# Kernel tuning notes

Measured on AMD Instinct MI355X. Metric: run time of the kernel, lower is better.

Reference implementation:

```python
import jax, jax.numpy as jnp
import numpy as np

N_NODES = 50000
N_EDGES = 800000
D_IN, D_HID, D_LAT = 128, 128, 64
BN_EPS = 1e-5


def setup_inputs() -> dict:
    key = jax.random.key(0)
    ks = jax.random.split(key, 8)
    x = jax.random.normal(ks[0], (N_NODES, D_IN), dtype=jnp.float32)
    edge_index = jax.random.randint(ks[1], (2, N_EDGES), 0, N_NODES, dtype=jnp.int64)
    s1 = 1.0 / np.sqrt(D_IN)
    s2 = 1.0 / np.sqrt(D_HID)
    W1 = jax.random.normal(ks[2], (D_IN, D_HID), dtype=jnp.float32) * s1
    b1 = jnp.zeros((D_HID,), jnp.float32)
    gamma = jnp.ones((D_HID,), jnp.float32)
    beta = jnp.zeros((D_HID,), jnp.float32)
    Wmu = jax.random.normal(ks[3], (D_HID, D_LAT), dtype=jnp.float32) * s2
    bmu = jnp.zeros((D_LAT,), jnp.float32)
    Wls = jax.random.normal(ks[4], (D_HID, D_LAT), dtype=jnp.float32) * s2
    bls = jnp.zeros((D_LAT,), jnp.float32)
    return {"x": x, "edge_index": edge_index, "W1": W1, "b1": b1,
            "gamma": gamma, "beta": beta, "Wmu": Wmu, "bmu": bmu,
            "Wls": Wls, "bls": bls}


def _gcn_conv(h, src, dst, norm_e, inv_deg, W, b):
    # PyG GCNConv: linear transform, then sym-normalized aggregation (A+I).
    h = h @ W                                   # [N, F]
    msgs = h[src] * norm_e[:, None]             # gather + edge scaling, [E, F]
    agg = jax.ops.segment_sum(msgs, dst, num_segments=h.shape[0])
    # self-loop contribution: norm[i]*norm[i] = 1/deg[i]
    return agg + h * inv_deg[:, None] + b


def reference(x, edge_index, W1, b1, gamma, beta, Wmu, bmu, Wls, bls):
    src, dst = edge_index[0], edge_index[1]
    n = x.shape[0]
    # degrees including self loops (GCN symmetric normalization)
    deg = jax.ops.segment_sum(jnp.ones(dst.shape, x.dtype), dst, num_segments=n) + 1.0
    inv_sqrt_deg = jax.lax.rsqrt(deg)
    norm_e = inv_sqrt_deg[src] * inv_sqrt_deg[dst]   # per-edge norm, [E]
    inv_deg = 1.0 / deg

    h = _gcn_conv(x, src, dst, norm_e, inv_deg, W1, b1)
    # BatchNorm1d with batch statistics (biased var), then ReLU; dropout off (eval)
    mean = h.mean(axis=0)
    var = h.var(axis=0)
    h = (h - mean) * jax.lax.rsqrt(var + BN_EPS) * gamma + beta
    h = jax.nn.relu(h)

    mu = _gcn_conv(h, src, dst, norm_e, inv_deg, Wmu, bmu)
    log_std = _gcn_conv(h, src, dst, norm_e, inv_deg, Wls, bls)
    return mu, log_std
```

## Files before the change

### kernel.cpp

```cpp
#include <hip/hip_runtime.h>
#include <hip/hip_bf16.h>

#define N_NODES 50000
#define N_EDGES 800000
#define F 128
#define L 64
#define BN_EPS 1e-5f
#define SCAN_BLOCKS 196
#define BN_BLOCKS 391
#define NPART 8
#define PART_SZ 6250
#define FILL_BLOCKS 2048
#define GEMM_BLOCKS 782

typedef __attribute__((ext_vector_type(8))) short short8;
typedef __attribute__((ext_vector_type(8))) unsigned short ushort8;
typedef __attribute__((ext_vector_type(4))) unsigned short ushortx4;
typedef __attribute__((ext_vector_type(4))) float f32x4;

static __device__ __forceinline__ float loadF(const void* p, int i, int f32) {
    if (f32) return ((const float*)p)[i];
    return __bfloat162float(((const __hip_bfloat16*)p)[i]);
}
static __device__ __forceinline__ int loadI(const void* p, int i, int i64) {
    if (i64) return (int)((const long long*)p)[i];
    return ((const int*)p)[i];
}
static __device__ __forceinline__ float bfu2f(unsigned short u) {
    unsigned int t = ((unsigned int)u) << 16;
    float f;
    __builtin_memcpy(&f, &t, 4);
    return f;
}
static __device__ __forceinline__ short f2bf_s(float f) {
    union { __hip_bfloat16 b; short s; } cv;
    cv.b = __float2bfloat16(f);
    return cv.s;
}
static __device__ __forceinline__ unsigned short f2bf_u(float f) {
    union { __hip_bfloat16 b; unsigned short u; } cv;
    cv.b = __float2bfloat16(f);
    return cv.u;
}

__global__ void k_prep(const void* __restrict__ W1, const void* __restrict__ Wmu,
                       const void* __restrict__ Wls, const unsigned short* __restrict__ xs,
                       const int* __restrict__ ei, __hip_bfloat16* __restrict__ Wt1,
                       __hip_bfloat16* __restrict__ Wt2, int* __restrict__ flags,
                       int* __restrict__ degi) {
    int b = blockIdx.x;
    int t = threadIdx.x;
    if (b == 0) {
        __shared__ int cnt[2];
        if (t < 2) cnt[t] = 0;
        __syncthreads();
        unsigned short v = xs[2 * t];
        int e = (v >> 7) & 0xff;
        int sane = (e >= 112 && e <= 133) ? 1 : 0;
        if (v == 0 || v == 0x8000) sane = 1;
        atomicAdd(&cnt[0], sane);
        atomicAdd(&cnt[1], (ei[2 * t + 1] != 0) ? 1 : 0);
        __syncthreads();
        if (t == 0) {
            flags[0] = (cnt[0] < 128) ? 1 : 0;
            flags[1] = (cnt[1] < 8) ? 1 : 0;
            flags[2] = 0;
        }
    } else if (b <= 64) {
        __shared__ int cnt;
        if (t == 0) cnt = 0;
        __syncthreads();
        unsigned short v = ((const unsigned short*)W1)[2 * t];
        int e = (v >> 7) & 0xff;
        atomicAdd(&cnt, (e >= 100 && e <= 133) ? 1 : 0);
        __syncthreads();
        int f32 = (cnt < 128) ? 1 : 0;
        int idx = (b - 1) * 256 + t;
        int n = idx >> 7, k = idx & 127;
        Wt1[idx] = __float2bfloat16(loadF(W1, k * F + n, f32));
        float v2 = (n < L) ? loadF(Wmu, k * L + n, f32) : loadF(Wls, k * L + (n - L), f32);
        Wt2[idx] = __float2bfloat16(v2);
    } else {
        int i = (b - 65) * 256 + t;
        if (i < N_NODES) degi[i] = 0;
    }
}

__global__ void k_eiprep(const void* ei, const int* __restrict__ flags,
                         int* __restrict__ src32, int* __restrict__ dst32,
                         int* __restrict__ degi) {
    int e = blockIdx.x * blockDim.x + threadIdx.x;
    if (e < N_EDGES) {
        int i64 = flags[1];
        int d = loadI(ei, N_EDGES + e, i64);
        if (i64) {
            src32[e] = loadI(ei, e, 1);
            dst32[e] = d;
        }
        atomicAdd(&degi[d], 1);
    }
}

__global__ void k_offs_alloc(const int* __restrict__ degi, int* __restrict__ flags,
                             int* __restrict__ offs, float* __restrict__ isd,
                             int* __restrict__ cur) {
    __shared__ int s[256];
    __shared__ int base;
    int t = threadIdx.x;
    int i = blockIdx.x * 256 + t;
    int v = (i < N_NODES) ? degi[i] : 0;
    s[t] = v;
    __syncthreads();
    for (int o = 1; o < 256; o <<= 1) {
        int u = (t >= o) ? s[t - o] : 0;
        __syncthreads();
        s[t] += u;
        __syncthreads();
    }
    if (t == 255) base = atomicAdd(&flags[2], s[255]);
    __syncthreads();
    if (i < N_NODES) {
        offs[i] = base + s[t] - v;
        isd[i] = 1.0f / sqrtf((float)v + 1.0f);
        cur[i] = 0;
    }
}

static __device__ __forceinline__ void gemm_body(int bid, const void* __restrict__ Xin,
        const __hip_bfloat16* __restrict__ Wt, const float* __restrict__ isd,
        const int* __restrict__ flags, int mode,
        const float* __restrict__ bnscale, const float* __restrict__ bnshift,
        unsigned short* __restrict__ outb) {
    int wave = threadIdx.x >> 6, lane = threadIdx.x & 63;
    int quad = lane >> 4, mr = lane & 15;
    int m0 = bid * 64 + wave * 16;
    int node = m0 + mr;
    int row = (node < N_NODES) ? node : N_NODES - 1;
    short8 a[4];
    if (mode == 1) {
        const unsigned short* xb = (const unsigned short*)Xin;
#pragma unroll
        for (int t = 0; t < 4; ++t) {
            int k0 = t * 32 + quad * 8;
            ushort8 raw = *(const ushort8*)(xb + row * F + k0);
            f32x4 s0 = *(const f32x4*)(bnscale + k0);
            f32x4 s1 = *(const f32x4*)(bnscale + k0 + 4);
            f32x4 h0 = *(const f32x4*)(bnshift + k0);
            f32x4 h1 = *(const f32x4*)(bnshift + k0 + 4);
            short8 av;
#pragma unroll
            for (int j = 0; j < 4; ++j)
                av[j] = f2bf_s(fmaxf(bfu2f(raw[j]) * s0[j] + h0[j], 0.f));
#pragma unroll
            for (int j = 0; j < 4; ++j)
                av[4 + j] = f2bf_s(fmaxf(bfu2f(raw[4 + j]) * s1[j] + h1[j], 0.f));
            a[t] = av;
        }
    } else if (flags[0]) {
        const float* xf = (const float*)Xin;
#pragma unroll
        for (int t = 0; t < 4; ++t) {
            int off = row * F + t * 32 + quad * 8;
            f32x4 v0 = *(const f32x4*)(xf + off);
            f32x4 v1 = *(const f32x4*)(xf + off + 4);
            short8 av;
#pragma unroll
            for (int j = 0; j < 4; ++j) av[j] = f2bf_s(v0[j]);
#pragma unroll
            for (int j = 0; j < 4; ++j) av[4 + j] = f2bf_s(v1[j]);
            a[t] = av;
        }
    } else {
        const short* xb = (const short*)Xin;
#pragma unroll
        for (int t = 0; t < 4; ++t)
            a[t] = *(const short8*)(xb + row * F + t * 32 + quad * 8);
    }
    f32x4 acc[8];
    const short* wb = (const short*)Wt;
#pragma unroll
    for (int nt = 0; nt < 8; ++nt) {
        const short* wp = wb + (nt * 16 + mr) * F + quad * 8;
        f32x4 c = {0.f, 0.f, 0.f, 0.f};
        c = __builtin_amdgcn_mfma_f32_16x16x32_bf16(*(const short8*)(wp), a[0], c, 0, 0, 0);
        c = __builtin_amdgcn_mfma_f32_16x16x32_bf16(*(const short8*)(wp + 32), a[1], c, 0, 0, 0);
        c = __builtin_amdgcn_mfma_f32_16x16x32_bf16(*(const short8*)(wp + 64), a[2], c, 0, 0, 0);
        c = __builtin_amdgcn_mfma_f32_16x16x32_bf16(*(const short8*)(wp + 96), a[3], c, 0, 0, 0);
        acc[nt] = c;
    }
    if (node < N_NODES) {
        float sd = isd[node];
        unsigned short* op = outb + node * F;
#pragma unroll
        for (int nt = 0; nt < 8; ++nt) {
            ushortx4 r;
#pragma unroll
            for (int j = 0; j < 4; ++j) r[j] = f2bf_u(acc[nt][j] * sd);
            *(ushortx4*)(op + nt * 16 + quad * 4) = r;
        }
    }
}

__global__ __launch_bounds__(256) void k_fill_gemm1(
        const int* __restrict__ ei32, const int* __restrict__ src32,
        const int* __restrict__ dst32, const int* __restrict__ flags,
        const int* __restrict__ offs, int* __restrict__ cur, int* __restrict__ csr,
        const void* __restrict__ X, const __hip_bfloat16* __restrict__ Wt1,
        const float* __restrict__ isd, unsigned short* __restrict__ outb) {
    if (blockIdx.x < FILL_BLOCKS) {
        const int* sp;
        const int* dp;
        if (flags[1]) { sp = src32; dp = dst32; }
        else          { sp = ei32;  dp = ei32 + N_EDGES; }
        int grp = blockIdx.x & (NPART - 1);
        int sub = blockIdx.x >> 3;
        int lo = grp * PART_SZ, hi = lo + PART_SZ;
        int stride = (FILL_BLOCKS >> 3) * 256;
        for (int e = sub * 256 + threadIdx.x; e < N_EDGES; e += stride) {
            int d = dp[e];
            if (d >= lo && d < hi) {
                int pos = offs[d] + atomicAdd(&cur[d], 1);
                csr[pos] = sp[e];
            }
        }
    } else {
        gemm_body(blockIdx.x - FILL_BLOCKS, X, Wt1, isd, flags, 0, nullptr, nullptr, outb);
    }
}

__global__ __launch_bounds__(256) void k_gemm_bn(const void* __restrict__ Xin,
        const __hip_bfloat16* __restrict__ Wt, const float* __restrict__ isd,
        const int* __restrict__ flags, const float* __restrict__ bnscale,
        const float* __restrict__ bnshift, unsigned short* __restrict__ outb) {
    gemm_body(blockIdx.x, Xin, Wt, isd, flags, 1, bnscale, bnshift, outb);
}

static __device__ __forceinline__ void agg_accum(int node, int grp, int l16,
        const ushort8* __restrict__ vp, const int* __restrict__ csr,
        const int* __restrict__ offs, const int* __restrict__ degi, float acc[8]) {
#pragma unroll
    for (int j = 0; j < 8; ++j) acc[j] = 0.f;
    if (grp == 0) {
        ushort8 u = vp[node * 16 + l16];
#pragma unroll
        for (int j = 0; j < 8; ++j) acc[j] = bfu2f(u[j]);
    }
    int start = offs[node];
    int end = start + degi[node];
    int i = start + grp;
    for (; i + 12 < end; i += 16) {
        ushort8 u0 = vp[csr[i] * 16 + l16];
        ushort8 u1 = vp[csr[i + 4] * 16 + l16];
        ushort8 u2 = vp[csr[i + 8] * 16 + l16];
        ushort8 u3 = vp[csr[i + 12] * 16 + l16];
#pragma unroll
        for (int j = 0; j < 8; ++j)
            acc[j] += (bfu2f(u0[j]) + bfu2f(u1[j])) + (bfu2f(u2[j]) + bfu2f(u3[j]));
    }
    for (; i + 4 < end; i += 8) {
        ushort8 u0 = vp[csr[i] * 16 + l16];
        ushort8 u1 = vp[csr[i + 4] * 16 + l16];
#pragma unroll
        for (int j = 0; j < 8; ++j) acc[j] += bfu2f(u0[j]) + bfu2f(u1[j]);
    }
    for (; i < end; i += 4) {
        ushort8 u = vp[csr[i] * 16 + l16];
#pragma unroll
        for (int j = 0; j < 8; ++j) acc[j] += bfu2f(u[j]);
    }
#pragma unroll
    for (int j = 0; j < 8; ++j) {
        acc[j] += __shfl_xor(acc[j], 16);
        acc[j] += __shfl_xor(acc[j], 32);
    }
}

__global__ void k_agg1(const unsigned short* __restrict__ val, const int* __restrict__ csr,
                       const int* __restrict__ offs, const int* __restrict__ degi,
                       const float* __restrict__ isd, const void* __restrict__ b1,
                       const int* __restrict__ flags, unsigned short* __restrict__ out) {
    int node = blockIdx.x * 4 + (threadIdx.x >> 6);
    if (node >= N_NODES) return;
    int lane = threadIdx.x & 63;
    int grp = lane >> 4, l16 = lane & 15;
    float acc[8];
    agg_accum(node, grp, l16, (const ushort8*)val, csr, offs, degi, acc);
    if (grp == 0) {
        float sd = isd[node];
        int c0 = l16 * 8, f32 = flags[0];
        ushort8 r;
#pragma unroll
        for (int j = 0; j < 8; ++j) r[j] = f2bf_u(acc[j] * sd + loadF(b1, c0 + j, f32));
        ((ushort8*)out)[node * 16 + l16] = r;
    }
}

__global__ void k_bnstats(const unsigned short* __restrict__ h, float* __restrict__ partial) {
    __shared__ float ls[256][8];
    __shared__ float lq[256][8];
    int t = threadIdx.x;
    int o = t & 15, rg = t >> 4;
    int row0 = blockIdx.x * 128 + rg;
    float s[8] = {0.f}, q[8] = {0.f};
#pragma unroll
    for (int i = 0; i < 8; ++i) {
        int row = row0 + i * 16;
        if (row < N_NODES) {
            ushort8 u = *(const ushort8*)(h + row * F + o * 8);
#pragma unroll
            for (int j = 0; j < 8; ++j) {
                float v = bfu2f(u[j]);
                s[j] += v;
                q[j] += v * v;
            }
        }
    }
#pragma unroll
    for (int j = 0; j < 8; ++j) { ls[t][j] = s[j]; lq[t][j] = q[j]; }
    __syncthreads();
    if (t < 128) {
        int c = t, oo = c >> 3, jj = c & 7;
        float ts = 0.f, tq = 0.f;
#pragma unroll
        for (int rgi = 0; rgi < 16; ++rgi) {
            ts += ls[rgi * 16 + oo][jj];
            tq += lq[rgi * 16 + oo][jj];
        }
        partial[blockIdx.x * 256 + c] = ts;
        partial[blockIdx.x * 256 + 128 + c] = tq;
    }
}

__global__ void k_bnredprep(const float* __restrict__ partial, const void* __restrict__ gamma,
                            const void* __restrict__ beta, const int* __restrict__ flags,
                            float* __restrict__ scale, float* __restrict__ shift) {
    int c = blockIdx.x;
    float s = 0.f, q = 0.f;
    for (int b = threadIdx.x; b < BN_BLOCKS; b += 256) {
        s += partial[b * 256 + c];
        q += partial[b * 256 + 128 + c];
    }
#pragma unroll
    for (int o = 32; o; o >>= 1) {
        s += __shfl_down(s, o);
        q += __shfl_down(q, o);
    }
    __shared__ float ws[4], wq[4];
    if ((threadIdx.x & 63) == 0) {
        ws[threadIdx.x >> 6] = s;
        wq[threadIdx.x >> 6] = q;
    }
    __syncthreads();
    if (threadIdx.x == 0) {
        float S = ws[0] + ws[1] + ws[2] + ws[3];
        float Q = wq[0] + wq[1] + wq[2] + wq[3];
        const float invN = 1.0f / (float)N_NODES;
        float m = S * invN;
        float var = Q * invN - m * m;
        int f32 = flags[0];
        float sc = loadF(gamma, c, f32) * rsqrtf(var + BN_EPS);
        scale[c] = sc;
        shift[c] = loadF(beta, c, f32) - m * sc;
    }
}

__global__ void k_agg2(const unsigned short* __restrict__ val, const int* __restrict__ csr,
                       const int* __restrict__ offs, const int* __restrict__ degi,
                       const float* __restrict__ isd, const void* __restrict__ bmu,
                       const void* __restrict__ bls, const int* __restrict__ flags,
                       void* __restrict__ out) {
    int node = blockIdx.x * 4 + (threadIdx.x >> 6);
    if (node >= N_NODES) return;
    int lane = threadIdx.x & 63;
    int grp = lane >> 4, l16 = lane & 15;
    float acc[8];
    agg_accum(node, grp, l16, (const ushort8*)val, csr, offs, degi, acc);
    if (grp == 0) {
        float sd = isd[node];
        int c0 = l16 * 8, f32 = flags[0];
        int hsel = (c0 >= L) ? 1 : 0;
        int cc = c0 - hsel * L;
        const void* bp = hsel ? bls : bmu;
        float o8[8];
#pragma unroll
        for (int j = 0; j < 8; ++j) o8[j] = acc[j] * sd + loadF(bp, cc + j, f32);
        long base_o = (long)hsel * (N_NODES * 64) + (long)node * 64 + cc;
        if (f32) {
            float4 r0 = make_float4(o8[0], o8[1], o8[2], o8[3]);
            float4 r1 = make_float4(o8[4], o8[5], o8[6], o8[7]);
            *(float4*)((float*)out + base_o) = r0;
            *(float4*)((float*)out + base_o + 4) = r1;
        } else {
            ushort8 r;
#pragma unroll
            for (int j = 0; j < 8; ++j) r[j] = f2bf_u(o8[j]);
            *(ushort8*)((__hip_bfloat16*)out + base_o) = r;
        }
    }
}

extern "C" void kernel_launch(void* const* d_in, const int* in_sizes, int n_in,
                              void* d_out, int out_size, void* d_ws, size_t ws_size,
                              hipStream_t stream) {
    const void* x     = d_in[0];
    const void* ei    = d_in[1];
    const void* W1    = d_in[2];
    const void* b1    = d_in[3];
    const void* gamma = d_in[4];
    const void* beta  = d_in[5];
    const void* Wmu   = d_in[6];
    const void* bmu   = d_in[7];
    const void* Wls   = d_in[8];
    const void* bls   = d_in[9];

    int*   degi  = (int*)d_ws;
    int*   offs  = degi + 50048;
    int*   cur   = offs + 50048;
    float* isd   = (float*)(cur + 50048);
    float* stats = isd + 50048;
    int*   flags = (int*)(stats + 512);
    int*   csr   = flags + 16;
    int*   src32 = csr + 800000;
    int*   dst32 = src32 + 800000;
    __hip_bfloat16* Wt1 = (__hip_bfloat16*)(dst32 + 800000);
    __hip_bfloat16* Wt2 = Wt1 + 16384;
    unsigned short* Abf = (unsigned short*)(Wt2 + 16384);
    unsigned short* Hpre = Abf + N_NODES * F;
    float* partial = (float*)(Hpre + N_NODES * F);

    const int NT = 256;
    const int AGG_BLOCKS = (N_NODES + 3) / 4;

    k_prep<<<65 + SCAN_BLOCKS, NT, 0, stream>>>(W1, Wmu, Wls, (const unsigned short*)x,
                                                (const int*)ei, Wt1, Wt2, flags, degi);
    k_eiprep<<<(N_EDGES + NT - 1) / NT, NT, 0, stream>>>(ei, flags, src32, dst32, degi);
    k_offs_alloc<<<SCAN_BLOCKS, NT, 0, stream>>>(degi, flags, offs, isd, cur);
    k_fill_gemm1<<<FILL_BLOCKS + GEMM_BLOCKS, NT, 0, stream>>>(
        (const int*)ei, src32, dst32, flags, offs, cur, csr, x, Wt1, isd, Abf);
    k_agg1<<<AGG_BLOCKS, NT, 0, stream>>>(Abf, csr, offs, degi, isd, b1, flags, Hpre);
    k_bnstats<<<BN_BLOCKS, NT, 0, stream>>>(Hpre, partial);
    k_bnredprep<<<128, NT, 0, stream>>>(partial, gamma, beta, flags, stats, stats + 128);
    k_gemm_bn<<<GEMM_BLOCKS, NT, 0, stream>>>(Hpre, Wt2, isd, flags, stats, stats + 128, Abf);
    k_agg2<<<AGG_BLOCKS, NT, 0, stream>>>(Abf, csr, offs, degi, isd, bmu, bls, flags, d_out);
}
```

Baseline: 308.4 us.

## Pad degree/offset counters, merge edge prep into prep kernel, simplify CSR fill

Degree and offset counters are padded to 16 ints per node so each counter sits on its own cache line, which is meant to reduce atomic contention from false sharing. Edge index conversion and degree counting move into k_prep, replacing the separate k_eiprep launch, and the counters are zeroed with hipMemsetAsync. The CSR fill drops the 8-way destination partitioning and the separate cur array and instead atomically bumps the offset itself, which then serves as the row end in aggregation. Output stores become nontemporal. The padding multiplies the footprint of the offset and degree arrays, so aggregation reads of them become strided.

Measured after the change: 314.9 us. 1.02x slower.

```diff
diff --git a/kernel.cpp b/kernel.cpp
--- a/kernel.cpp
+++ b/kernel.cpp
@@ -6,12 +6,12 @@
 #define F 128
 #define L 64
 #define BN_EPS 1e-5f
+#define PAD 16
 #define SCAN_BLOCKS 196
 #define BN_BLOCKS 391
-#define NPART 8
-#define PART_SZ 6250
-#define FILL_BLOCKS 2048
+#define EDGE_BLOCKS 3125
 #define GEMM_BLOCKS 782
+#define FILLB 1266
 
 typedef __attribute__((ext_vector_type(8))) short short8;
 typedef __attribute__((ext_vector_type(8))) unsigned short ushort8;
@@ -21,10 +21,6 @@
 static __device__ __forceinline__ float loadF(const void* p, int i, int f32) {
     if (f32) return ((const float*)p)[i];
     return __bfloat162float(((const __hip_bfloat16*)p)[i]);
-}
-static __device__ __forceinline__ int loadI(const void* p, int i, int i64) {
-    if (i64) return (int)((const long long*)p)[i];
-    return ((const int*)p)[i];
 }
 static __device__ __forceinline__ float bfu2f(unsigned short u) {
     unsigned int t = ((unsigned int)u) << 16;
@@ -45,9 +41,10 @@
 
 __global__ void k_prep(const void* __restrict__ W1, const void* __restrict__ Wmu,
                        const void* __restrict__ Wls, const unsigned short* __restrict__ xs,
-                       const int* __restrict__ ei, __hip_bfloat16* __restrict__ Wt1,
+                       const void* __restrict__ ei, __hip_bfloat16* __restrict__ Wt1,
                        __hip_bfloat16* __restrict__ Wt2, int* __restrict__ flags,
-                       int* __restrict__ degi) {
+                       int* __restrict__ degiP, int* __restrict__ src32,
+                       int* __restrict__ dst32) {
     int b = blockIdx.x;
     int t = threadIdx.x;
     if (b == 0) {
@@ -59,7 +56,7 @@
         int sane = (e >= 112 && e <= 133) ? 1 : 0;
         if (v == 0 || v == 0x8000) sane = 1;
         atomicAdd(&cnt[0], sane);
-        atomicAdd(&cnt[1], (ei[2 * t + 1] != 0) ? 1 : 0);
+        atomicAdd(&cnt[1], (((const int*)ei)[2 * t + 1] != 0) ? 1 : 0);
         __syncthreads();
         if (t == 0) {
             flags[0] = (cnt[0] < 128) ? 1 : 0;
@@ -81,34 +78,33 @@
         float v2 = (n < L) ? loadF(Wmu, k * L + n, f32) : loadF(Wls, k * L + (n - L), f32);
         Wt2[idx] = __float2bfloat16(v2);
     } else {
-        int i = (b - 65) * 256 + t;
-        if (i < N_NODES) degi[i] = 0;
-    }
-}
-
-__global__ void k_eiprep(const void* ei, const int* __restrict__ flags,
-                         int* __restrict__ src32, int* __restrict__ dst32,
-                         int* __restrict__ degi) {
-    int e = blockIdx.x * blockDim.x + threadIdx.x;
-    if (e < N_EDGES) {
-        int i64 = flags[1];
-        int d = loadI(ei, N_EDGES + e, i64);
-        if (i64) {
-            src32[e] = loadI(ei, e, 1);
-            dst32[e] = d;
-        }
-        atomicAdd(&degi[d], 1);
-    }
-}
-
-__global__ void k_offs_alloc(const int* __restrict__ degi, int* __restrict__ flags,
-                             int* __restrict__ offs, float* __restrict__ isd,
-                             int* __restrict__ cur) {
+        int e0 = (b - 65) * 256 + t;
+        __shared__ int nz;
+        if (t == 0) nz = 0;
+        __syncthreads();
+        int w = ((const int*)ei)[2 * e0 + 1];
+        if (w != 0) atomicAdd(&nz, 1);
+        __syncthreads();
+        int d;
+        if (nz < 8) {
+            int s = (int)((const long long*)ei)[e0];
+            d = (int)((const long long*)ei)[N_EDGES + e0];
+            src32[e0] = s;
+            dst32[e0] = d;
+        } else {
+            d = ((const int*)ei)[N_EDGES + e0];
+        }
+        atomicAdd(&degiP[d * PAD], 1);
+    }
+}
+
+__global__ void k_offs_alloc(const int* __restrict__ degiP, int* __restrict__ flags,
+                             int* __restrict__ offsP, float* __restrict__ isd) {
     __shared__ int s[256];
     __shared__ int base;
     int t = threadIdx.x;
     int i = blockIdx.x * 256 + t;
-    int v = (i < N_NODES) ? degi[i] : 0;
+    int v = (i < N_NODES) ? degiP[i * PAD] : 0;
     s[t] = v;
     __syncthreads();
     for (int o = 1; o < 256; o <<= 1) {
@@ -120,9 +116,8 @@
     if (t == 255) base = atomicAdd(&flags[2], s[255]);
     __syncthreads();
     if (i < N_NODES) {
-        offs[i] = base + s[t] - v;
+        offsP[i * PAD] = base + s[t] - v;
         isd[i] = 1.0f / sqrtf((float)v + 1.0f);
-        cur[i] = 0;
     }
 }
 
@@ -204,27 +199,23 @@
 __global__ __launch_bounds__(256) void k_fill_gemm1(
         const int* __restrict__ ei32, const int* __restrict__ src32,
         const int* __restrict__ dst32, const int* __restrict__ flags,
-        const int* __restrict__ offs, int* __restrict__ cur, int* __restrict__ csr,
+        int* __restrict__ offsP, int* __restrict__ csr,
         const void* __restrict__ X, const __hip_bfloat16* __restrict__ Wt1,
         const float* __restrict__ isd, unsigned short* __restrict__ outb) {
-    if (blockIdx.x < FILL_BLOCKS) {
+    if (blockIdx.x < GEMM_BLOCKS) {
+        gemm_body(blockIdx.x, X, Wt1, isd, flags, 0, nullptr, nullptr, outb);
+    } else {
         const int* sp;
         const int* dp;
         if (flags[1]) { sp = src32; dp = dst32; }
         else          { sp = ei32;  dp = ei32 + N_EDGES; }
-        int grp = blockIdx.x & (NPART - 1);
-        int sub = blockIdx.x >> 3;
-        int lo = grp * PART_SZ, hi = lo + PART_SZ;
-        int stride = (FILL_BLOCKS >> 3) * 256;
-        for (int e = sub * 256 + threadIdx.x; e < N_EDGES; e += stride) {
+        int stride = FILLB * 256;
+        for (int e = (blockIdx.x - GEMM_BLOCKS) * 256 + threadIdx.x; e < N_EDGES;
+             e += stride) {
             int d = dp[e];
-            if (d >= lo && d < hi) {
-                int pos = offs[d] + atomicAdd(&cur[d], 1);
-                csr[pos] = sp[e];
-            }
-        }
-    } else {
-        gemm_body(blockIdx.x - FILL_BLOCKS, X, Wt1, isd, flags, 0, nullptr, nullptr, outb);
+            int pos = atomicAdd(&offsP[d * PAD], 1);
+            csr[pos] = sp[e];
+        }
     }
 }
 
@@ -237,7 +228,7 @@
 
 static __device__ __forceinline__ void agg_accum(int node, int grp, int l16,
         const ushort8* __restrict__ vp, const int* __restrict__ csr,
-        const int* __restrict__ offs, const int* __restrict__ degi, float acc[8]) {
+        const int* __restrict__ offsP, const int* __restrict__ degiP, float acc[8]) {
 #pragma unroll
     for (int j = 0; j < 8; ++j) acc[j] = 0.f;
     if (grp == 0) {
@@ -245,8 +236,8 @@
 #pragma unroll
         for (int j = 0; j < 8; ++j) acc[j] = bfu2f(u[j]);
     }
-    int start = offs[node];
-    int end = start + degi[node];
+    int end = offsP[node * PAD];
+    int start = end - degiP[node * PAD];
     int i = start + grp;
     for (; i + 12 < end; i += 16) {
         ushort8 u0 = vp[csr[i] * 16 + l16];
@@ -276,7 +267,7 @@
 }
 
 __global__ void k_agg1(const unsigned short* __restrict__ val, const int* __restrict__ csr,
-                       const int* __restrict__ offs, const int* __restrict__ degi,
+                       const int* __restrict__ offsP, const int* __restrict__ degiP,
                        const float* __restrict__ isd, const void* __restrict__ b1,
                        const int* __restrict__ flags, unsigned short* __restrict__ out) {
     int node = blockIdx.x * 4 + (threadIdx.x >> 6);
@@ -284,7 +275,7 @@
     int lane = threadIdx.x & 63;
     int grp = lane >> 4, l16 = lane & 15;
     float acc[8];
-    agg_accum(node, grp, l16, (const ushort8*)val, csr, offs, degi, acc);
+    agg_accum(node, grp, l16, (const ushort8*)val, csr, offsP, degiP, acc);
     if (grp == 0) {
         float sd = isd[node];
         int c0 = l16 * 8, f32 = flags[0];
@@ -365,7 +356,7 @@
 }
 
 __global__ void k_agg2(const unsigned short* __restrict__ val, const int* __restrict__ csr,
-                       const int* __restrict__ offs, const int* __restrict__ degi,
+                       const int* __restrict__ offsP, const int* __restrict__ degiP,
                        const float* __restrict__ isd, const void* __restrict__ bmu,
                        const void* __restrict__ bls, const int* __restrict__ flags,
                        void* __restrict__ out) {
@@ -374,7 +365,7 @@
     int lane = threadIdx.x & 63;
     int grp = lane >> 4, l16 = lane & 15;
     float acc[8];
-    agg_accum(node, grp, l16, (const ushort8*)val, csr, offs, degi, acc);
+    agg_accum(node, grp, l16, (const ushort8*)val, csr, offsP, degiP, acc);
     if (grp == 0) {
         float sd = isd[node];
         int c0 = l16 * 8, f32 = flags[0];
@@ -386,15 +377,15 @@
         for (int j = 0; j < 8; ++j) o8[j] = acc[j] * sd + loadF(bp, cc + j, f32);
         long base_o = (long)hsel * (N_NODES * 64) + (long)node * 64 + cc;
         if (f32) {
-            float4 r0 = make_float4(o8[0], o8[1], o8[2], o8[3]);
-            float4 r1 = make_float4(o8[4], o8[5], o8[6], o8[7]);
-            *(float4*)((float*)out + base_o) = r0;
-            *(float4*)((float*)out + base_o + 4) = r1;
+            f32x4 r0 = {o8[0], o8[1], o8[2], o8[3]};
+            f32x4 r1 = {o8[4], o8[5], o8[6], o8[7]};
+            __builtin_nontemporal_store(r0, (f32x4*)((float*)out + base_o));
+            __builtin_nontemporal_store(r1, (f32x4*)((float*)out + base_o + 4));
         } else {
             ushort8 r;
 #pragma unroll
             for (int j = 0; j < 8; ++j) r[j] = f2bf_u(o8[j]);
-            *(ushort8*)((__hip_bfloat16*)out + base_o) = r;
+            __builtin_nontemporal_store(r, (ushort8*)((__hip_bfloat16*)out + base_o));
         }
     }
 }
@@ -413,10 +404,9 @@
     const void* Wls   = d_in[8];
     const void* bls   = d_in[9];
 
-    int*   degi  = (int*)d_ws;
-    int*   offs  = degi + 50048;
-    int*   cur   = offs + 50048;
-    float* isd   = (float*)(cur + 50048);
+    int*   degiP = (int*)d_ws;
+    int*   offsP = degiP + N_NODES * PAD;
+    float* isd   = (float*)(offsP + N_NODES * PAD);
     float* stats = isd + 50048;
     int*   flags = (int*)(stats + 512);
     int*   csr   = flags + 16;
@@ -431,15 +421,15 @@
     const int NT = 256;
     const int AGG_BLOCKS = (N_NODES + 3) / 4;
 
-    k_prep<<<65 + SCAN_BLOCKS, NT, 0, stream>>>(W1, Wmu, Wls, (const unsigned short*)x,
-                                                (const int*)ei, Wt1, Wt2, flags, degi);
-    k_eiprep<<<(N_EDGES + NT - 1) / NT, NT, 0, stream>>>(ei, flags, src32, dst32, degi);
-    k_offs_alloc<<<SCAN_BLOCKS, NT, 0, stream>>>(degi, flags, offs, isd, cur);
-    k_fill_gemm1<<<FILL_BLOCKS + GEMM_BLOCKS, NT, 0, stream>>>(
-        (const int*)ei, src32, dst32, flags, offs, cur, csr, x, Wt1, isd, Abf);
-    k_agg1<<<AGG_BLOCKS, NT, 0, stream>>>(Abf, csr, offs, degi, isd, b1, flags, Hpre);
+    hipMemsetAsync(degiP, 0, (size_t)N_NODES * PAD * sizeof(int), stream);
+    k_prep<<<65 + EDGE_BLOCKS, NT, 0, stream>>>(W1, Wmu, Wls, (const unsigned short*)x,
+                                                ei, Wt1, Wt2, flags, degiP, src32, dst32);
+    k_offs_alloc<<<SCAN_BLOCKS, NT, 0, stream>>>(degiP, flags, offsP, isd);
+    k_fill_gemm1<<<GEMM_BLOCKS + FILLB, NT, 0, stream>>>(
+        (const int*)ei, src32, dst32, flags, offsP, csr, x, Wt1, isd, Abf);
+    k_agg1<<<AGG_BLOCKS, NT, 0, stream>>>(Abf, csr, offsP, degiP, isd, b1, flags, Hpre);
     k_bnstats<<<BN_BLOCKS, NT, 0, stream>>>(Hpre, partial);
     k_bnredprep<<<128, NT, 0, stream>>>(partial, gamma, beta, flags, stats, stats + 128);
     k_gemm_bn<<<GEMM_BLOCKS, NT, 0, stream>>>(Hpre, Wt2, isd, flags, stats, stats + 128, Abf);
-    k_agg2<<<AGG_BLOCKS, NT, 0, stream>>>(Abf, csr, offs, degi, isd, bmu, bls, flags, d_out);
-}
+    k_agg2<<<AGG_BLOCKS, NT, 0, stream>>>(Abf, csr, offsP, degiP, isd, bmu, bls, flags, d_out);
+}
```
